# Kernel optimization log

Hardware: AMD Instinct MI355X
Metric: run time of the kernel (lower is better)

The kernel has to match this reference:

```python
import jax, jax.numpy as jnp
import numpy as np

SCALING = 2.0  # lora scaling attached via set_lora (lora_alpha / r)


def setup_inputs() -> dict:
    key = jax.random.key(0)
    ks = jax.random.split(key, 8)
    E, DIN, DOUT, N, K, R = 8, 2048, 2048, 4096, 2, 16
    inputs = jax.random.normal(ks[0], (N, DIN), jnp.float32)
    weight = jax.random.normal(ks[1], (E, DOUT, DIN), jnp.float32) * 0.02
    lora_A = jax.random.normal(ks[2], (E, R, DIN), jnp.float32) * 0.02
    lora_B = jax.random.normal(ks[3], (E, DOUT, R), jnp.float32) * 0.02
    gates = jax.nn.softmax(jax.random.normal(ks[4], (N, K), jnp.float32), axis=-1)
    # expert assignment per (token, slot); scattermoe contract:
    #   sorted_scattered_idxs = argsort(assign); token = idx // k, slot = idx % k
    assign = jax.random.randint(ks[5], (N * K,), 0, E)
    sorted_scattered_idxs = jnp.argsort(assign).astype(jnp.int32)
    sorted_expert_idxs = assign[sorted_scattered_idxs].astype(jnp.int32)
    counts = jnp.bincount(assign, length=E)
    expert_offsets = jnp.cumsum(counts).astype(jnp.int32)
    return dict(inputs=inputs, weight=weight, lora_A=lora_A, lora_B=lora_B,
                gates=gates, sorted_expert_idxs=sorted_expert_idxs,
                sorted_scattered_idxs=sorted_scattered_idxs,
                expert_offsets=expert_offsets, k=K)


def reference(inputs, weight, lora_A, lora_B, gates, sorted_expert_idxs,
              sorted_scattered_idxs, expert_offsets, k):
    # Fused LoRA grouped GEMM:  Y = X @ W + scaling * (X @ A^T) @ B^T
    # grouped_in=False, grouped_out=False, bias=None (module defaults).
    E = weight.shape[0]
    N = gates.shape[0]
    W = jnp.swapaxes(weight, 1, 2)          # [E, din, dout] (weight.permute(0,2,1))
    token = sorted_scattered_idxs // k      # source token per sorted slot
    slot = sorted_scattered_idxs % k        # which of the k routes
    x = inputs[token]                       # gather -> [N*k, din]
    y = jnp.zeros((x.shape[0], W.shape[2]), x.dtype)
    for e in range(E):                      # fixed small expert loop
        m = (sorted_expert_idxs == e)[:, None]
        xe = jnp.where(m, x, 0.0)
        y = y + (xe @ W[e] + SCALING * ((xe @ jnp.swapaxes(lora_A[e], 0, 1)) @ jnp.swapaxes(lora_B[e], 0, 1)))
    g = gates[token, slot][:, None]         # gate per sorted slot
    out = jnp.zeros((N, W.shape[2]), y.dtype).at[token].add(y * g)
    return out
```

## Files before the change

kernel.cpp:

```cpp
#include <hip/hip_runtime.h>
#include <hip/hip_bf16.h>

#define E_    8
#define DIN   2048
#define DOUT  2048
#define N_TOK 4096
#define NK    8192
#define R_    16
#define KEXT  2112
#define KT_N  (KEXT / 64)

typedef __bf16 bf16x8 __attribute__((ext_vector_type(8)));
typedef float  f32x4  __attribute__((ext_vector_type(4)));
typedef unsigned short u16x8 __attribute__((ext_vector_type(8)));

static __device__ __forceinline__ void gld16(const void* g, void* l) {
  __builtin_amdgcn_global_load_lds(
      (const __attribute__((address_space(1))) unsigned int*)g,
      (__attribute__((address_space(3))) unsigned int*)l, 16, 0, 0);
}

static __device__ __forceinline__ unsigned short f2bfu(float f) {
  union { float f; unsigned int u; } v; v.f = f;
  unsigned int r = v.u + 0x7fffu + ((v.u >> 16) & 1u);
  return (unsigned short)(r >> 16);
}

__global__ void __launch_bounds__(64)
k_wconv(const float* __restrict__ w, const float* __restrict__ lb,
        unsigned short* __restrict__ wbe) {
  const long long row = blockIdx.x;
  const float4* src  = (const float4*)(w + row * DIN);
  const float4* lsrc = (const float4*)(lb + row * R_);
  ushort4* dst = (ushort4*)(wbe + row * KEXT);
  for (int u = threadIdx.x; u < KEXT / 4; u += 64) {
    float4 v;
    if (u < 512)       v = src[u];
    else if (u < 516)  v = lsrc[u - 512];
    else               v = make_float4(0.f, 0.f, 0.f, 0.f);
    ushort4 o;
    o.x = f2bfu(v.x); o.y = f2bfu(v.y); o.z = f2bfu(v.z); o.w = f2bfu(v.w);
    dst[u] = o;
  }
}

__global__ void k_aconv(const float* __restrict__ a, unsigned short* __restrict__ ab) {
  long long i = (long long)blockIdx.x * blockDim.x + threadIdx.x;
  float4 v = ((const float4*)a)[i];
  ushort4 o;
  o.x = f2bfu(v.x); o.y = f2bfu(v.y); o.z = f2bfu(v.z); o.w = f2bfu(v.w);
  ((ushort4*)ab)[i] = o;
}

__global__ void k_gather(const float* __restrict__ x, const int* __restrict__ ssi,
                         const float* __restrict__ gates, const int* __restrict__ kptr,
                         unsigned short* __restrict__ Xe, float* __restrict__ gate,
                         int* __restrict__ tok) {
  int s = blockIdx.x;
  int ssv = ssi[s];
  int kk = kptr[0];
  int t = ssv / kk, sl = ssv - t * kk;
  if (threadIdx.x == 0) { gate[s] = gates[t * kk + sl]; tok[s] = t; }
  const float4* src = (const float4*)(x + (long long)t * DIN);
  ushort4* dst = (ushort4*)(Xe + (long long)s * KEXT);
  for (int i = threadIdx.x; i < 512; i += 256) {
    float4 v = src[i];
    ushort4 o;
    o.x = f2bfu(v.x); o.y = f2bfu(v.y); o.z = f2bfu(v.z); o.w = f2bfu(v.w);
    dst[i] = o;
  }
  if (threadIdx.x < 12) {
    ushort4 z; z.x = z.y = z.z = z.w = 0;
    dst[516 + threadIdx.x] = z;
  }
}

__global__ void __launch_bounds__(64)
k_xa(unsigned short* __restrict__ Xe, const unsigned short* __restrict__ Ab,
     const int* __restrict__ eoff) {
  int tile = blockIdx.x;
  int off_prev = 0, e = -1, m_start = 0, m_end = 0, acc_t = 0;
#pragma unroll
  for (int i = 0; i < E_; i++) {
    int oe = eoff[i];
    int te = (oe - off_prev + 15) >> 4;
    if (e < 0 && tile < acc_t + te) {
      e = i; m_start = off_prev + (tile - acc_t) * 16; m_end = oe;
    }
    acc_t += te; off_prev = oe;
  }
  if (e < 0) return;
  const int lane = threadIdx.x;
  const int l15 = lane & 15, quad = lane >> 4;
  int arow = m_start + l15; if (arow >= m_end) arow = m_end - 1;
  const unsigned short* xp = Xe + (long long)arow * KEXT + quad * 8;
  const unsigned short* bp = Ab + ((long long)e * R_ + l15) * DIN + quad * 8;
  f32x4 acc = (f32x4){0.f, 0.f, 0.f, 0.f};
#pragma unroll 8
  for (int k0 = 0; k0 < DIN; k0 += 32) {
    bf16x8 a = *(const bf16x8*)(xp + k0);
    bf16x8 b = *(const bf16x8*)(bp + k0);
    acc = __builtin_amdgcn_mfma_f32_16x16x32_bf16(a, b, acc, 0, 0, 0);
  }
#pragma unroll
  for (int t = 0; t < 4; t++) {
    int slot = m_start + quad * 4 + t;
    if (slot < m_end)
      Xe[(long long)slot * KEXT + 2048 + l15] = f2bfu(2.0f * acc[t]);
  }
}

__global__ void __launch_bounds__(256)
k_gemm(const unsigned short* __restrict__ Xe, const unsigned short* __restrict__ Wbe,
       const float* __restrict__ gate, const int* __restrict__ tok,
       const int* __restrict__ eoff, float* __restrict__ out) {
  __shared__ alignas(16) unsigned short sAB[2 * 128 * 64];
  __shared__ float gs[128];
  __shared__ int   ts[128];

  const int id = blockIdx.x;
  const int xcd = id & 7, local = id >> 3;
  const int mt = local % 72;
  const int nt = (xcd << 1) | (local / 72);
  const int n_start = nt << 7;

  int off_prev = 0, e = -1, m_start = 0, m_end = 0, acc_t = 0;
#pragma unroll
  for (int i = 0; i < E_; i++) {
    int oe = eoff[i];
    int te = (oe - off_prev + 127) >> 7;
    if (e < 0 && mt < acc_t + te) {
      e = i; m_start = off_prev + (mt - acc_t) * 128; m_end = oe;
    }
    acc_t += te;
    off_prev = oe;
  }
  if (e < 0) return;

  const int tid = threadIdx.x;
  const int w = tid >> 6, lane = tid & 63;
  const int wm = w & 1, wn = w >> 1;
  const int quad = lane >> 4, l15 = lane & 15;

  if (tid < 128) {
    int gm = m_start + tid; if (gm >= m_end) gm = m_end - 1;
    gs[tid] = gate[gm];
    ts[tid] = tok[gm];
  }

  f32x4 acc[4][4];
#pragma unroll
  for (int mi = 0; mi < 4; mi++)
#pragma unroll
    for (int ni = 0; ni < 4; ni++)
      acc[mi][ni] = (f32x4){0.f, 0.f, 0.f, 0.f};

  const int srow = lane >> 3;
  const int scol = ((lane & 7) ^ srow) * 8;
  const unsigned short* Wbase = Wbe + (long long)e * DOUT * KEXT;

  for (int kt = 0; kt < KT_N; kt++) {
    const int k0 = kt * 64;
#pragma unroll
    for (int j = 0; j < 4; j++) {
      int c = w * 4 + j;
      int rt = c * 8 + srow;
      int ga = m_start + rt; if (ga >= m_end) ga = m_end - 1;
      gld16(Xe + (long long)ga * KEXT + k0 + scol, &sAB[c * 512 + lane * 8]);
      gld16(Wbase + (long long)(n_start + rt) * KEXT + k0 + scol,
            &sAB[8192 + c * 512 + lane * 8]);
    }
    __syncthreads();
#pragma unroll
    for (int ks = 0; ks < 2; ks++) {
      const int kx = (((ks << 2) | quad) ^ (l15 & 7)) << 3;
      bf16x8 af[4], bfr[4];
#pragma unroll
      for (int mi = 0; mi < 4; mi++)
        af[mi] = *(const bf16x8*)&sAB[(wm * 64 + mi * 16 + l15) * 64 + kx];
#pragma unroll
      for (int ni = 0; ni < 4; ni++)
        bfr[ni] = *(const bf16x8*)&sAB[8192 + (wn * 64 + ni * 16 + l15) * 64 + kx];
#pragma unroll
      for (int mi = 0; mi < 4; mi++)
#pragma unroll
        for (int ni = 0; ni < 4; ni++)
          acc[mi][ni] = __builtin_amdgcn_mfma_f32_16x16x32_bf16(
              af[mi], bfr[ni], acc[mi][ni], 0, 0, 0);
    }
    __syncthreads();
  }

#pragma unroll
  for (int ni = 0; ni < 4; ni++) {
    int n = n_start + wn * 64 + ni * 16 + l15;
#pragma unroll
    for (int mi = 0; mi < 4; mi++) {
#pragma unroll
      for (int t4 = 0; t4 < 4; t4++) {
        int row = wm * 64 + mi * 16 + quad * 4 + t4;
        if (m_start + row >= m_end) continue;
        float o = acc[mi][ni][t4] * gs[row];
        atomicAdd(out + (long long)ts[row] * DOUT + n, o);
      }
    }
  }
}

extern "C" void kernel_launch(void* const* d_in, const int* in_sizes, int n_in,
                              void* d_out, int out_size, void* d_ws, size_t ws_size,
                              hipStream_t stream) {
  (void)in_sizes; (void)n_in; (void)out_size; (void)ws_size;
  const float* inputs = (const float*)d_in[0];
  const float* weight = (const float*)d_in[1];
  const float* lora_A = (const float*)d_in[2];
  const float* lora_B = (const float*)d_in[3];
  const float* gates  = (const float*)d_in[4];
  const int* sei  = (const int*)d_in[5];
  const int* ssi  = (const int*)d_in[6];
  const int* eoff = (const int*)d_in[7];
  const int* kptr = (const int*)d_in[8];
  (void)sei;
  float* out = (float*)d_out;

  unsigned char* ws = (unsigned char*)d_ws;
  unsigned short* Wbe = (unsigned short*)ws;
  unsigned short* Xe  = (unsigned short*)(ws + 69206016);
  unsigned short* Ab  = (unsigned short*)(ws + 103809024);
  float* gate = (float*)(ws + 104333312);
  int*   tok  = (int*)(ws + 104366080);

  hipMemsetAsync(d_out, 0, (size_t)N_TOK * DOUT * sizeof(float), stream);
  k_wconv<<<E_ * DOUT, 64, 0, stream>>>(weight, lora_B, Wbe);
  k_aconv<<<256, 256, 0, stream>>>(lora_A, Ab);
  k_gather<<<NK, 256, 0, stream>>>(inputs, ssi, gates, kptr, Xe, gate, tok);
  k_xa<<<519, 64, 0, stream>>>(Xe, Ab, eoff);
  k_gemm<<<1152, 256, 0, stream>>>(Xe, Wbe, gate, tok, eoff, out);
}
```

Before: 435.2 us.

## Fuse gather/convert with LoRA X·A^T projection and widen weight-conversion blocks

Merges the token gather + bf16 conversion kernel with the LoRA down-projection kernel: each 64-thread block gathers its 16 rows into padded LDS, writes them to the Xe buffer, and computes X·A^T from LDS instead of re-reading Xe from global memory. This removes one launch and a global re-read. The trade-off is that the gather now runs on only about 520 single-wavefront blocks, each looping serially over 16 rows, so parallelism is far lower than the old 8192-block gather. Separately, the weight conversion kernel now packs four rows into one 256-thread block.

```diff
diff --git a/kernel.cpp b/kernel.cpp
--- a/kernel.cpp
+++ b/kernel.cpp
@@ -9,6 +9,7 @@
 #define R_    16
 #define KEXT  2112
 #define KT_N  (KEXT / 64)
+#define XROW_PAD 2052
 
 typedef __bf16 bf16x8 __attribute__((ext_vector_type(8)));
 typedef float  f32x4  __attribute__((ext_vector_type(4)));
@@ -26,14 +27,15 @@
   return (unsigned short)(r >> 16);
 }
 
-__global__ void __launch_bounds__(64)
+__global__ void __launch_bounds__(256)
 k_wconv(const float* __restrict__ w, const float* __restrict__ lb,
         unsigned short* __restrict__ wbe) {
-  const long long row = blockIdx.x;
+  const long long row = (long long)blockIdx.x * 4 + (threadIdx.x >> 6);
+  const int lane = threadIdx.x & 63;
   const float4* src  = (const float4*)(w + row * DIN);
   const float4* lsrc = (const float4*)(lb + row * R_);
   ushort4* dst = (ushort4*)(wbe + row * KEXT);
-  for (int u = threadIdx.x; u < KEXT / 4; u += 64) {
+  for (int u = lane; u < KEXT / 4; u += 64) {
     float4 v;
     if (u < 512)       v = src[u];
     else if (u < 516)  v = lsrc[u - 512];
@@ -52,32 +54,14 @@
   ((ushort4*)ab)[i] = o;
 }
 
-__global__ void k_gather(const float* __restrict__ x, const int* __restrict__ ssi,
-                         const float* __restrict__ gates, const int* __restrict__ kptr,
-                         unsigned short* __restrict__ Xe, float* __restrict__ gate,
-                         int* __restrict__ tok) {
-  int s = blockIdx.x;
-  int ssv = ssi[s];
-  int kk = kptr[0];
-  int t = ssv / kk, sl = ssv - t * kk;
-  if (threadIdx.x == 0) { gate[s] = gates[t * kk + sl]; tok[s] = t; }
-  const float4* src = (const float4*)(x + (long long)t * DIN);
-  ushort4* dst = (ushort4*)(Xe + (long long)s * KEXT);
-  for (int i = threadIdx.x; i < 512; i += 256) {
-    float4 v = src[i];
-    ushort4 o;
-    o.x = f2bfu(v.x); o.y = f2bfu(v.y); o.z = f2bfu(v.z); o.w = f2bfu(v.w);
-    dst[i] = o;
-  }
-  if (threadIdx.x < 12) {
-    ushort4 z; z.x = z.y = z.z = z.w = 0;
-    dst[516 + threadIdx.x] = z;
-  }
-}
-
 __global__ void __launch_bounds__(64)
-k_xa(unsigned short* __restrict__ Xe, const unsigned short* __restrict__ Ab,
-     const int* __restrict__ eoff) {
+k_prep_x(const float* __restrict__ x, const unsigned short* __restrict__ Ab,
+         const int* __restrict__ ssi, const float* __restrict__ gates,
+         const int* __restrict__ kptr, const int* __restrict__ eoff,
+         unsigned short* __restrict__ Xe, float* __restrict__ gate,
+         int* __restrict__ tok) {
+  __shared__ alignas(16) unsigned short lx[16 * XROW_PAD];
+
   int tile = blockIdx.x;
   int off_prev = 0, e = -1, m_start = 0, m_end = 0, acc_t = 0;
 #pragma unroll
@@ -90,15 +74,40 @@
     acc_t += te; off_prev = oe;
   }
   if (e < 0) return;
+
   const int lane = threadIdx.x;
+  const int kk = kptr[0];
   const int l15 = lane & 15, quad = lane >> 4;
-  int arow = m_start + l15; if (arow >= m_end) arow = m_end - 1;
-  const unsigned short* xp = Xe + (long long)arow * KEXT + quad * 8;
+
+  for (int r = 0; r < 16; r++) {
+    int slot = m_start + r;
+    bool valid = slot < m_end;
+    int src_slot = valid ? slot : (m_end - 1);
+    int ssv = ssi[src_slot];
+    int t = ssv / kk, sl = ssv - t * kk;
+    const float4* srow = (const float4*)(x + (long long)t * DIN);
+    ushort4* drow = (ushort4*)(Xe + (long long)slot * KEXT);
+#pragma unroll
+    for (int i2 = 0; i2 < 8; i2++) {
+      int u = lane + i2 * 64;
+      float4 v = srow[u];
+      ushort4 o;
+      o.x = f2bfu(v.x); o.y = f2bfu(v.y); o.z = f2bfu(v.z); o.w = f2bfu(v.w);
+      *(ushort4*)&lx[r * XROW_PAD + u * 4] = o;
+      if (valid) drow[u] = o;
+    }
+    if (valid) {
+      if (lane == 0) { gate[slot] = gates[t * kk + sl]; tok[slot] = t; }
+      if (lane < 12) { ushort4 z; z.x = z.y = z.z = z.w = 0; drow[516 + lane] = z; }
+    }
+  }
+  __syncthreads();
+
   const unsigned short* bp = Ab + ((long long)e * R_ + l15) * DIN + quad * 8;
   f32x4 acc = (f32x4){0.f, 0.f, 0.f, 0.f};
-#pragma unroll 8
+#pragma unroll 4
   for (int k0 = 0; k0 < DIN; k0 += 32) {
-    bf16x8 a = *(const bf16x8*)(xp + k0);
+    bf16x8 a = *(const bf16x8*)&lx[l15 * XROW_PAD + k0 + quad * 8];
     bf16x8 b = *(const bf16x8*)(bp + k0);
     acc = __builtin_amdgcn_mfma_f32_16x16x32_bf16(a, b, acc, 0, 0, 0);
   }
@@ -231,9 +240,8 @@
   int*   tok  = (int*)(ws + 104366080);
 
   hipMemsetAsync(d_out, 0, (size_t)N_TOK * DOUT * sizeof(float), stream);
-  k_wconv<<<E_ * DOUT, 64, 0, stream>>>(weight, lora_B, Wbe);
+  k_wconv<<<E_ * DOUT / 4, 256, 0, stream>>>(weight, lora_B, Wbe);
   k_aconv<<<256, 256, 0, stream>>>(lora_A, Ab);
-  k_gather<<<NK, 256, 0, stream>>>(inputs, ssi, gates, kptr, Xe, gate, tok);
-  k_xa<<<519, 64, 0, stream>>>(Xe, Ab, eoff);
+  k_prep_x<<<520, 64, 0, stream>>>(inputs, Ab, ssi, gates, kptr, eoff, Xe, gate, tok);
   k_gemm<<<1152, 256, 0, stream>>>(Xe, Wbe, gate, tok, eoff, out);
 }
```

After: 510.4 us. 1.17x slower.
